# Kernel optimization log

Measured on AMD Instinct MI355X. Metric: run time of the kernel, lower is better.

The kernel has to match this reference:

```python
import jax, jax.numpy as jnp
import numpy as np
import math

D_MODEL = 1024
N_HEADS = 16
D_K = 64
D_V = 64
B = 4
S = 1024


def setup_inputs() -> dict:
    key = jax.random.key(0)
    ks = jax.random.split(key, 11)
    # xavier-ish init scale for projections
    s_in = 1.0 / math.sqrt(D_MODEL)
    return {
        "queries": jax.random.normal(ks[0], (B, S, D_MODEL), jnp.float32),
        "keys": jax.random.normal(ks[1], (B, S, D_MODEL), jnp.float32),
        "values": jax.random.normal(ks[2], (B, S, D_MODEL), jnp.float32),
        "Wq": jax.random.normal(ks[3], (D_MODEL, N_HEADS * D_K), jnp.float32) * s_in,
        "bq": jnp.zeros((N_HEADS * D_K,), jnp.float32),
        "Wk": jax.random.normal(ks[4], (D_MODEL, N_HEADS * D_K), jnp.float32) * s_in,
        "bk": jnp.zeros((N_HEADS * D_K,), jnp.float32),
        "Wv": jax.random.normal(ks[5], (D_MODEL, N_HEADS * D_V), jnp.float32) * s_in,
        "bv": jnp.zeros((N_HEADS * D_V,), jnp.float32),
        "Wo": jax.random.normal(ks[6], (N_HEADS * D_V, D_MODEL), jnp.float32) * (1.0 / math.sqrt(N_HEADS * D_V)),
        "bo": jnp.zeros((D_MODEL,), jnp.float32),
    }


def reference(queries, keys, values, Wq, bq, Wk, bk, Wv, bv, Wo, bo):
    Bq, Sq, _ = queries.shape
    Sk = keys.shape[1]
    scale = 1.0 / math.sqrt(D_K)
    # projections -> [B, S, H, d]
    q = (queries @ Wq + bq).reshape(Bq, Sq, N_HEADS, D_K)
    k = (keys @ Wk + bk).reshape(Bq, Sk, N_HEADS, D_K)
    v = (values @ Wv + bv).reshape(Bq, Sk, N_HEADS, D_V)
    # scaled dot-product attention: scores [B, H, Sq, Sk]
    scores = jnp.einsum("bqhd,bkhd->bhqk", q, k) * scale
    attn = jax.nn.softmax(scores, axis=-1)
    # weighted values -> [B, Sq, H*D_V]
    out = jnp.einsum("bhqk,bkhd->bqhd", attn, v).reshape(Bq, Sq, N_HEADS * D_V)
    return out @ Wo + bo
```

## Files before the change

### kernel.cpp

```cpp
#include <hip/hip_runtime.h>
#include <hip/hip_bf16.h>

typedef __attribute__((ext_vector_type(4))) float f32x4;
typedef __attribute__((ext_vector_type(16))) float f32x16;
typedef __attribute__((ext_vector_type(8))) short bf16x8;
typedef __attribute__((ext_vector_type(4))) unsigned short u16x4;
typedef __attribute__((ext_vector_type(8))) unsigned short u16x8;
typedef __attribute__((ext_vector_type(2))) unsigned int u32x2;

#define MFMA16(a, b, c) __builtin_amdgcn_mfma_f32_16x16x32_bf16((a), (b), (c), 0, 0, 0)
#define MFMA32(a, b, c) __builtin_amdgcn_mfma_f32_32x32x16_bf16((a), (b), (c), 0, 0, 0)

static __device__ __forceinline__ unsigned short f2bf(float f) {
    union { float f; unsigned int u; } v; v.f = f;
    unsigned int r = v.u + 0x7FFFu + ((v.u >> 16) & 1u);
    return (unsigned short)(r >> 16);
}
static __device__ __forceinline__ unsigned int pk2(float x, float y) {
    unsigned int r;
    asm("v_cvt_pk_bf16_f32 %0, %1, %2" : "=v"(r) : "v"(x), "v"(y));
    return r;
}

static __device__ __forceinline__ void gload_lds16(const void* g, void* l) {
    __builtin_amdgcn_global_load_lds(
        (const __attribute__((address_space(1))) void*)g,
        (__attribute__((address_space(3))) void*)l, 16, 0, 0);
}

__global__ __launch_bounds__(256) void convert_act(
    const float* __restrict__ q, const float* __restrict__ k,
    const float* __restrict__ v, unsigned short* __restrict__ qc,
    unsigned short* __restrict__ kc, unsigned short* __restrict__ vc) {
    const float* src = blockIdx.y == 0 ? q : (blockIdx.y == 1 ? k : v);
    unsigned short* dst = blockIdx.y == 0 ? qc : (blockIdx.y == 1 ? kc : vc);
    size_t off = ((size_t)blockIdx.x * 256 + threadIdx.x) * 8;
    f32x4 a = *(const f32x4*)&src[off];
    f32x4 b = *(const f32x4*)&src[off + 4];
    union { unsigned int u[4]; u16x8 v; } o;
    o.u[0] = pk2(a[0], a[1]); o.u[1] = pk2(a[2], a[3]);
    o.u[2] = pk2(b[0], b[1]); o.u[3] = pk2(b[2], b[3]);
    *(u16x8*)&dst[off] = o.v;
}

__global__ __launch_bounds__(256) void transpose_w(
    const float* __restrict__ Wq, const float* __restrict__ Wk,
    const float* __restrict__ Wv, const float* __restrict__ Wo,
    unsigned short* __restrict__ Wt_all, unsigned short* __restrict__ Wot) {
    __shared__ unsigned short T[64][65];
    const int z = blockIdx.z;
    const float* W = z == 0 ? Wq : (z == 1 ? Wk : (z == 2 ? Wv : Wo));
    unsigned short* Wt = z < 3 ? (Wt_all + (size_t)z * 1024 * 1024) : Wot;
    const int k0 = blockIdx.y * 64, n0 = blockIdx.x * 64;
    const int t = threadIdx.x;
    const int rl = t >> 4, c4 = (t & 15) * 4;
#pragma unroll
    for (int i = 0; i < 4; ++i) {
        f32x4 v = *(const f32x4*)&W[(size_t)(k0 + rl + 16 * i) * 1024 + n0 + c4];
#pragma unroll
        for (int j = 0; j < 4; ++j) T[rl + 16 * i][c4 + j] = f2bf(v[j]);
    }
    __syncthreads();
#pragma unroll
    for (int i = 0; i < 4; ++i) {
        u16x4 o;
#pragma unroll
        for (int j = 0; j < 4; ++j) o[j] = T[c4 + j][rl + 16 * i];
        *(u16x4*)&Wt[(size_t)(n0 + rl + 16 * i) * 1024 + k0 + c4] = o;
    }
}

template <bool OUT_BF16, int BN>
__global__ __launch_bounds__(256, 2) void gemm_fast(
    const unsigned short* __restrict__ A0, const unsigned short* __restrict__ A1,
    const unsigned short* __restrict__ A2, const unsigned short* __restrict__ Wt,
    const float* __restrict__ b0, const float* __restrict__ b1,
    const float* __restrict__ b2, void* __restrict__ Outv, int ldo) {
    constexpr int NF = BN / 32;
    __shared__ __align__(16) unsigned short As[128 * 32];
    __shared__ __align__(16) unsigned short Bs[BN * 32];

    const int t = threadIdx.x;
    const int w = t >> 6, lane = t & 63;
    const int wr = w >> 1, wc = w & 1;
    const int g = lane >> 4, r15 = lane & 15;
    const int bm = blockIdx.y * 128;
    const int bn = blockIdx.x * BN;
    const int msel = bn >> 10;
    const unsigned short* A = msel == 0 ? A0 : (msel == 1 ? A1 : A2);
    const float* bias = msel == 0 ? b0 : (msel == 1 ? b1 : b2);
    const int l4 = lane >> 2, c8 = (lane & 3) * 8;

    f32x4 acc[4][NF];
#pragma unroll
    for (int m = 0; m < 4; ++m)
#pragma unroll
        for (int n = 0; n < NF; ++n) acc[m][n] = (f32x4){0.f, 0.f, 0.f, 0.f};

    for (int kt = 0; kt < 1024; kt += 32) {
        __syncthreads();
        gload_lds16(&A[(size_t)(bm + 16 * w + l4) * 1024 + kt + c8], &As[w * 512]);
        gload_lds16(&A[(size_t)(bm + 16 * (w + 4) + l4) * 1024 + kt + c8], &As[(w + 4) * 512]);
        if (BN == 128) {
            gload_lds16(&Wt[(size_t)(bn + 16 * w + l4) * 1024 + kt + c8], &Bs[w * 512]);
            gload_lds16(&Wt[(size_t)(bn + 16 * (w + 4) + l4) * 1024 + kt + c8],
                        &Bs[(w + 4) * 512 % (BN * 32)]);
        } else {
            gload_lds16(&Wt[(size_t)(bn + 16 * w + l4) * 1024 + kt + c8], &Bs[w * 512]);
        }
        __syncthreads();
        bf16x8 af[4], bfr[NF];
#pragma unroll
        for (int m = 0; m < 4; ++m)
            af[m] = *(const bf16x8*)&As[(wr * 64 + m * 16 + r15) * 32 + g * 8];
#pragma unroll
        for (int n = 0; n < NF; ++n)
            bfr[n] = *(const bf16x8*)&Bs[(wc * (BN / 2) + n * 16 + r15) * 32 + g * 8];
#pragma unroll
        for (int m = 0; m < 4; ++m)
#pragma unroll
            for (int n = 0; n < NF; ++n)
                acc[m][n] = MFMA16(af[m], bfr[n], acc[m][n]);
    }

    float* Of = (float*)Outv;
    unsigned short* Ob = (unsigned short*)Outv;
#pragma unroll
    for (int n = 0; n < NF; ++n) {
        int col = bn + wc * (BN / 2) + n * 16 + r15;
        float bv = bias[col & 1023];
#pragma unroll
        for (int m = 0; m < 4; ++m) {
#pragma unroll
            for (int r = 0; r < 4; ++r) {
                int row = bm + wr * 64 + m * 16 + g * 4 + r;
                float val = acc[m][n][r] + bv;
                if (OUT_BF16)
                    Ob[(size_t)row * ldo + col] = f2bf(val);
                else
                    Of[(size_t)row * ldo + col] = val;
            }
        }
    }
}

template <bool A_BF16, bool OUT_BF16>
__global__ __launch_bounds__(256, 2) void gemm_kernel(
    const void* __restrict__ Av, const float* __restrict__ W,
    const float* __restrict__ bias, void* __restrict__ Outv) {
    __shared__ __align__(16) unsigned short As[128][40];
    __shared__ __align__(16) unsigned short Bs[128][40];

    const int t = threadIdx.x;
    const int bm = blockIdx.y * 128;
    const int bn = blockIdx.x * 128;
    const int w = t >> 6, lane = t & 63;
    const int wr = w >> 1, wc = w & 1;
    const int g = lane >> 4, r15 = lane & 15;

    f32x4 acc[4][4];
#pragma unroll
    for (int m = 0; m < 4; ++m)
#pragma unroll
        for (int n = 0; n < 4; ++n) acc[m][n] = (f32x4){0.f, 0.f, 0.f, 0.f};

    const float* Af = (const float*)Av;
    const unsigned short* Ab = (const unsigned short*)Av;

    for (int kt = 0; kt < 1024; kt += 32) {
        __syncthreads();
#pragma unroll
        for (int i = 0; i < 4; ++i) {
            int row = (t >> 3) + i * 32;
            int c4 = (t & 7) * 4;
            if (A_BF16) {
                u16x4 v = *(const u16x4*)&Ab[(size_t)(bm + row) * 1024 + kt + c4];
                *(u16x4*)&As[row][c4] = v;
            } else {
                f32x4 v = *(const f32x4*)&Af[(size_t)(bm + row) * 1024 + kt + c4];
                u16x4 o;
                o[0] = f2bf(v[0]); o[1] = f2bf(v[1]);
                o[2] = f2bf(v[2]); o[3] = f2bf(v[3]);
                *(u16x4*)&As[row][c4] = o;
            }
        }
#pragma unroll
        for (int i = 0; i < 4; ++i) {
            int k = (t >> 5) + i * 8;
            int c4 = (t & 31) * 4;
            f32x4 v = *(const f32x4*)&W[(size_t)(kt + k) * 1024 + bn + c4];
#pragma unroll
            for (int j = 0; j < 4; ++j) Bs[c4 + j][k] = f2bf(v[j]);
        }
        __syncthreads();
        bf16x8 af[4], bfr[4];
#pragma unroll
        for (int m = 0; m < 4; ++m)
            af[m] = *(const bf16x8*)&As[wr * 64 + m * 16 + r15][g * 8];
#pragma unroll
        for (int n = 0; n < 4; ++n)
            bfr[n] = *(const bf16x8*)&Bs[wc * 64 + n * 16 + r15][g * 8];
#pragma unroll
        for (int m = 0; m < 4; ++m)
#pragma unroll
            for (int n = 0; n < 4; ++n)
                acc[m][n] = MFMA16(af[m], bfr[n], acc[m][n]);
    }

    float* Of = (float*)Outv;
    unsigned short* Ob = (unsigned short*)Outv;
#pragma unroll
    for (int n = 0; n < 4; ++n) {
        int col = bn + wc * 64 + n * 16 + r15;
        float bv = bias[col];
#pragma unroll
        for (int m = 0; m < 4; ++m) {
#pragma unroll
            for (int r = 0; r < 4; ++r) {
                int row = bm + wr * 64 + m * 16 + g * 4 + r;
                float val = acc[m][n][r] + bv;
                if (OUT_BF16)
                    Ob[(size_t)row * 1024 + col] = f2bf(val);
                else
                    Of[(size_t)row * 1024 + col] = val;
            }
        }
    }
}

__global__ __launch_bounds__(256, 2) void attn32_kernel(
    const unsigned short* __restrict__ Q, const unsigned short* __restrict__ K,
    const unsigned short* __restrict__ V, unsigned short* __restrict__ O, int ld) {
    __shared__ __align__(16) unsigned short Kls[2][64 * 80];
    __shared__ __align__(16) unsigned short Vls[2][64 * 80];

    const int t = threadIdx.x;
    const int w = t >> 6, lane = t & 63;
    const int q5 = lane & 31, hi = lane >> 5;

    const int id = blockIdx.x;
    const int sid = (id & 7) * 64 + (id >> 3);
    const int bh = sid >> 3, qb = sid & 7;
    const int b = bh >> 4, h = bh & 15;
    const int brow = b * 1024;
    const int q0 = qb * 128;

    const float c2 = 0.18033688f;

    const unsigned short* Qrow = Q + (size_t)(brow + q0 + w * 32 + q5) * ld + h * 64;
    bf16x8 qreg[8];
#pragma unroll
    for (int j = 0; j < 8; ++j) qreg[j] = *(const bf16x8*)&Qrow[8 * j];
    bf16x8 qsel[4];
#pragma unroll
    for (int kk = 0; kk < 4; ++kk) qsel[kk] = hi ? qreg[2 * kk + 1] : qreg[2 * kk];

    const int krow = t >> 2, kpart = t & 3;
    const int vp = t & 31, vdc = t >> 5;
    const unsigned short* Kg = K + h * 64;
    const unsigned short* Vg = V + h * 64;

    u16x8 kr0, kr1, vr0, vr1;
#define STG_LOAD(KT)                                                            \
    {                                                                           \
        size_t kro = (size_t)(brow + (KT) + krow) * ld;                         \
        kr0 = *(const u16x8*)&Kg[kro + kpart * 8];                              \
        kr1 = *(const u16x8*)&Kg[kro + kpart * 8 + 32];                         \
        size_t vro = (size_t)(brow + (KT) + 2 * vp) * ld;                       \
        vr0 = *(const u16x8*)&Vg[vro + vdc * 8];                                \
        vr1 = *(const u16x8*)&Vg[vro + ld + vdc * 8];                           \
    }
#define STG_WRITE(BUF)                                                          \
    {                                                                           \
        char* kb_ = (char*)Kls[BUF];                                            \
        int tg_ = (krow & 7) << 4;                                              \
        *(u16x8*)(kb_ + krow * 160 + ((kpart * 16) ^ tg_)) = kr0;               \
        *(u16x8*)(kb_ + krow * 160 + (((kpart + 4) * 16) ^ tg_)) = kr1;         \
        char* vb_ = (char*)Vls[BUF];                                            \
        _Pragma("unroll") for (int j_ = 0; j_ < 8; ++j_) {                      \
            int d_ = vdc * 8 + j_;                                              \
            unsigned int pk_ = (unsigned int)(unsigned short)vr0[j_] |          \
                               ((unsigned int)(unsigned short)vr1[j_] << 16);   \
            *(unsigned int*)(vb_ + d_ * 160 + ((vp * 4) ^ ((d_ & 7) << 4)))     \
                = pk_;                                                          \
        }                                                                       \
    }

    f32x16 acc0 = {}, acc1 = {};
    float mrun = -1e30f, lrun = 0.f;

    STG_LOAD(0);
    STG_WRITE(0);
    __syncthreads();

    int cur = 0;
    for (int tile = 0; tile < 16; ++tile) {
        const bool more = tile < 15;
        if (more) STG_LOAD(tile * 64 + 64);

        char* kb = (char*)Kls[cur];
        f32x16 st0 = {}, st1 = {};
        {
            const int tg0 = (q5 & 7) << 4;
            char* kp0 = kb + q5 * 160;
            char* kp1 = kb + (q5 + 32) * 160;
            __builtin_amdgcn_s_setprio(1);
#pragma unroll
            for (int kk = 0; kk < 4; ++kk) {
                int so = ((2 * kk + hi) * 16) ^ tg0;
                bf16x8 kf0 = *(const bf16x8*)(kp0 + so);
                bf16x8 kf1 = *(const bf16x8*)(kp1 + so);
                st0 = MFMA32(kf0, qsel[kk], st0);
                st1 = MFMA32(kf1, qsel[kk], st1);
            }
            __builtin_amdgcn_s_setprio(0);
        }

        float mloc = fmaxf(st0[0], st0[1]);
#pragma unroll
        for (int r = 2; r < 16; ++r) mloc = fmaxf(mloc, st0[r]);
#pragma unroll
        for (int r = 0; r < 16; ++r) mloc = fmaxf(mloc, st1[r]);
        mloc = fmaxf(mloc, __shfl_xor(mloc, 32));
        if (!__all(mloc - mrun <= 64.f)) {
            float mnew = fmaxf(mrun, mloc);
            float sf = exp2f((mrun - mnew) * c2);
            mrun = mnew;
            lrun *= sf;
#pragma unroll
            for (int r = 0; r < 16; ++r) { acc0[r] *= sf; acc1[r] *= sf; }
        }
        float mneg = -mrun * c2;
        float rs = 0.f;
#pragma unroll
        for (int r = 0; r < 16; ++r) {
            st0[r] = exp2f(fmaf(st0[r], c2, mneg));
            rs += st0[r];
        }
#pragma unroll
        for (int r = 0; r < 16; ++r) {
            st1[r] = exp2f(fmaf(st1[r], c2, mneg));
            rs += st1[r];
        }
        rs += __shfl_xor(rs, 32);
        lrun += rs;

        char* vb = (char*)Vls[cur];
        const int tgv = (q5 & 7) << 4;
        char* vp0 = vb + q5 * 160;
        char* vp1 = vb + (q5 + 32) * 160;
        __builtin_amdgcn_s_setprio(1);
#define PV_HALF(ST, CT)                                                         \
    _Pragma("unroll") for (int ks = 0; ks < 2; ++ks) {                          \
        unsigned int a0 = pk2(ST[8 * ks + 0], ST[8 * ks + 1]);                  \
        unsigned int a1 = pk2(ST[8 * ks + 2], ST[8 * ks + 3]);                  \
        unsigned int a2 = pk2(ST[8 * ks + 4], ST[8 * ks + 5]);                  \
        unsigned int a3 = pk2(ST[8 * ks + 6], ST[8 * ks + 7]);                  \
        unsigned int x0 = __shfl_xor(a0, 32), x1 = __shfl_xor(a1, 32);          \
        unsigned int x2 = __shfl_xor(a2, 32), x3 = __shfl_xor(a3, 32);          \
        union { unsigned int u[4]; bf16x8 v; } pfu;                             \
        pfu.u[0] = hi ? x2 : a0;                                                \
        pfu.u[1] = hi ? x3 : a1;                                                \
        pfu.u[2] = hi ? a2 : x0;                                                \
        pfu.u[3] = hi ? a3 : x1;                                                \
        int co = ((32 * (2 * (CT) + ks) + 16 * hi)) ^ tgv;                      \
        bf16x8 vf0 = *(const bf16x8*)(vp0 + co);                                \
        bf16x8 vf1 = *(const bf16x8*)(vp1 + co);                                \
        acc0 = MFMA32(vf0, pfu.v, acc0);                                        \
        acc1 = MFMA32(vf1, pfu.v, acc1);                                        \
    }
        PV_HALF(st0, 0);
        PV_HALF(st1, 1);
        __builtin_amdgcn_s_setprio(0);

        if (more) STG_WRITE(cur ^ 1);
        __syncthreads();
        cur ^= 1;
    }

    const float inv = 1.0f / lrun;
    unsigned short* Orow = O + (size_t)(brow + q0 + w * 32 + q5) * 1024 + h * 64;
#pragma unroll
    for (int k = 0; k < 4; ++k) {
        int d0 = 8 * k + 4 * hi;
        u32x2 pa, pb;
        pa[0] = pk2(acc0[4 * k + 0] * inv, acc0[4 * k + 1] * inv);
        pa[1] = pk2(acc0[4 * k + 2] * inv, acc0[4 * k + 3] * inv);
        *(u32x2*)&Orow[d0] = pa;
        pb[0] = pk2(acc1[4 * k + 0] * inv, acc1[4 * k + 1] * inv);
        pb[1] = pk2(acc1[4 * k + 2] * inv, acc1[4 * k + 3] * inv);
        *(u32x2*)&Orow[32 + d0] = pb;
    }
#undef STG_LOAD
#undef STG_WRITE
#undef PV_HALF
}

extern "C" void kernel_launch(void* const* d_in, const int* in_sizes, int n_in,
                              void* d_out, int out_size, void* d_ws, size_t ws_size,
                              hipStream_t stream) {
    const float* q  = (const float*)d_in[0];
    const float* k  = (const float*)d_in[1];
    const float* v  = (const float*)d_in[2];
    const float* Wq = (const float*)d_in[3];
    const float* bq = (const float*)d_in[4];
    const float* Wk = (const float*)d_in[5];
    const float* bk = (const float*)d_in[6];
    const float* Wv = (const float*)d_in[7];
    const float* bv = (const float*)d_in[8];
    const float* Wo = (const float*)d_in[9];
    const float* bo = (const float*)d_in[10];

    const size_t M1 = (size_t)1024 * 1024;
    const size_t NEED = 28 * M1 * sizeof(unsigned short);

    dim3 bt(256, 1, 1);
    if (ws_size >= NEED) {
        unsigned short* qc  = (unsigned short*)d_ws;
        unsigned short* kc  = qc + 4 * M1;
        unsigned short* vc  = kc + 4 * M1;
        unsigned short* Wt  = vc + 4 * M1;
        unsigned short* Wot = Wt + 3 * M1;
        unsigned short* QKV = Wot + M1;
        unsigned short* Ob  = qc;

        convert_act<<<dim3(2048, 3), bt, 0, stream>>>(q, k, v, qc, kc, vc);
        transpose_w<<<dim3(16, 16, 4), bt, 0, stream>>>(Wq, Wk, Wv, Wo, Wt, Wot);
        gemm_fast<true, 128><<<dim3(24, 32), bt, 0, stream>>>(qc, kc, vc, Wt, bq, bk, bv, QKV, 3072);
        attn32_kernel<<<dim3(512), bt, 0, stream>>>(QKV, QKV + 1024, QKV + 2048, Ob, 3072);
        gemm_fast<false, 64><<<dim3(16, 32), bt, 0, stream>>>(Ob, Ob, Ob, Wot, bo, bo, bo, d_out, 1024);
    } else {
        const size_t NE = (size_t)4096 * 1024;
        unsigned short* Qb = (unsigned short*)d_ws;
        unsigned short* Kb = Qb + NE;
        unsigned short* Vb = Kb + NE;
        unsigned short* Ob = Vb + NE;
        dim3 gg(8, 32);
        gemm_kernel<false, true><<<gg, bt, 0, stream>>>(q, Wq, bq, Qb);
        gemm_kernel<false, true><<<gg, bt, 0, stream>>>(k, Wk, bk, Kb);
        gemm_kernel<false, true><<<gg, bt, 0, stream>>>(v, Wv, bv, Vb);
        attn32_kernel<<<dim3(512), bt, 0, stream>>>(Qb, Kb, Vb, Ob, 1024);
        gemm_kernel<true, false><<<gg, bt, 0, stream>>>(Ob, Wo, bo, d_out);
    }
}
```

Before: 217.6 us.

## Split attention over KV halves with merge, double-buffer GEMMs, fuse prepass kernels

Fuses activation conversion and weight transpose into one prepass launch. Double-buffers the GEMM LDS staging so the next K-tile loads while the current one computes, adds MFMA priority hints, and retiles the output projection to BM=64 rows and 128 columns. Splits attention across two KV halves to double the grid to 1024 blocks, writing partial outputs plus max/sum stats that a new merge kernel combines. The split adds an extra launch, extra memory traffic and a second bf16 rounding of the partial outputs, and the small-workspace fallback path is removed.

```diff
diff --git a/kernel.cpp b/kernel.cpp
--- a/kernel.cpp
+++ b/kernel.cpp
@@ -21,6 +21,9 @@
     asm("v_cvt_pk_bf16_f32 %0, %1, %2" : "=v"(r) : "v"(x), "v"(y));
     return r;
 }
+static __device__ __forceinline__ float bf2f(unsigned short u) {
+    return __uint_as_float((unsigned int)u << 16);
+}
 
 static __device__ __forceinline__ void gload_lds16(const void* g, void* l) {
     __builtin_amdgcn_global_load_lds(
@@ -28,112 +31,126 @@
         (__attribute__((address_space(3))) void*)l, 16, 0, 0);
 }
 
-__global__ __launch_bounds__(256) void convert_act(
+__global__ __launch_bounds__(256) void prepass(
     const float* __restrict__ q, const float* __restrict__ k,
-    const float* __restrict__ v, unsigned short* __restrict__ qc,
-    unsigned short* __restrict__ kc, unsigned short* __restrict__ vc) {
-    const float* src = blockIdx.y == 0 ? q : (blockIdx.y == 1 ? k : v);
-    unsigned short* dst = blockIdx.y == 0 ? qc : (blockIdx.y == 1 ? kc : vc);
-    size_t off = ((size_t)blockIdx.x * 256 + threadIdx.x) * 8;
-    f32x4 a = *(const f32x4*)&src[off];
-    f32x4 b = *(const f32x4*)&src[off + 4];
-    union { unsigned int u[4]; u16x8 v; } o;
-    o.u[0] = pk2(a[0], a[1]); o.u[1] = pk2(a[2], a[3]);
-    o.u[2] = pk2(b[0], b[1]); o.u[3] = pk2(b[2], b[3]);
-    *(u16x8*)&dst[off] = o.v;
-}
-
-__global__ __launch_bounds__(256) void transpose_w(
-    const float* __restrict__ Wq, const float* __restrict__ Wk,
-    const float* __restrict__ Wv, const float* __restrict__ Wo,
-    unsigned short* __restrict__ Wt_all, unsigned short* __restrict__ Wot) {
+    const float* __restrict__ v, const float* __restrict__ Wq,
+    const float* __restrict__ Wk, const float* __restrict__ Wv,
+    const float* __restrict__ Wo, unsigned short* __restrict__ qc,
+    unsigned short* __restrict__ kc, unsigned short* __restrict__ vc,
+    unsigned short* __restrict__ Wt, unsigned short* __restrict__ Wot) {
     __shared__ unsigned short T[64][65];
-    const int z = blockIdx.z;
-    const float* W = z == 0 ? Wq : (z == 1 ? Wk : (z == 2 ? Wv : Wo));
-    unsigned short* Wt = z < 3 ? (Wt_all + (size_t)z * 1024 * 1024) : Wot;
-    const int k0 = blockIdx.y * 64, n0 = blockIdx.x * 64;
-    const int t = threadIdx.x;
-    const int rl = t >> 4, c4 = (t & 15) * 4;
-#pragma unroll
-    for (int i = 0; i < 4; ++i) {
-        f32x4 v = *(const f32x4*)&W[(size_t)(k0 + rl + 16 * i) * 1024 + n0 + c4];
-#pragma unroll
-        for (int j = 0; j < 4; ++j) T[rl + 16 * i][c4 + j] = f2bf(v[j]);
-    }
-    __syncthreads();
-#pragma unroll
-    for (int i = 0; i < 4; ++i) {
-        u16x4 o;
-#pragma unroll
-        for (int j = 0; j < 4; ++j) o[j] = T[c4 + j][rl + 16 * i];
-        *(u16x4*)&Wt[(size_t)(n0 + rl + 16 * i) * 1024 + k0 + c4] = o;
-    }
-}
-
-template <bool OUT_BF16, int BN>
+    const int id = blockIdx.x, t = threadIdx.x;
+    if (id < 6144) {
+        const int z = id >> 11;
+        const float* src = z == 0 ? q : (z == 1 ? k : v);
+        unsigned short* dst = z == 0 ? qc : (z == 1 ? kc : vc);
+        size_t off = ((size_t)(id & 2047) * 256 + t) * 8;
+        f32x4 a = *(const f32x4*)&src[off];
+        f32x4 b = *(const f32x4*)&src[off + 4];
+        union { unsigned int u[4]; u16x8 v; } o;
+        o.u[0] = pk2(a[0], a[1]); o.u[1] = pk2(a[2], a[3]);
+        o.u[2] = pk2(b[0], b[1]); o.u[3] = pk2(b[2], b[3]);
+        *(u16x8*)&dst[off] = o.v;
+    } else {
+        int r = id - 6144;
+        const int z = r >> 8; r &= 255;
+        const float* W = z == 0 ? Wq : (z == 1 ? Wk : (z == 2 ? Wv : Wo));
+        unsigned short* Wd = z < 3 ? (Wt + (size_t)z * 1024 * 1024) : Wot;
+        const int k0 = (r >> 4) * 64, n0 = (r & 15) * 64;
+        const int rl = t >> 4, c4 = (t & 15) * 4;
+#pragma unroll
+        for (int i = 0; i < 4; ++i) {
+            f32x4 vv = *(const f32x4*)&W[(size_t)(k0 + rl + 16 * i) * 1024 + n0 + c4];
+#pragma unroll
+            for (int j = 0; j < 4; ++j) T[rl + 16 * i][c4 + j] = f2bf(vv[j]);
+        }
+        __syncthreads();
+#pragma unroll
+        for (int i = 0; i < 4; ++i) {
+            u16x4 o;
+#pragma unroll
+            for (int j = 0; j < 4; ++j) o[j] = T[c4 + j][rl + 16 * i];
+            *(u16x4*)&Wd[(size_t)(n0 + rl + 16 * i) * 1024 + k0 + c4] = o;
+        }
+    }
+}
+
+template <bool OUT_BF16, int BM>
 __global__ __launch_bounds__(256, 2) void gemm_fast(
     const unsigned short* __restrict__ A0, const unsigned short* __restrict__ A1,
     const unsigned short* __restrict__ A2, const unsigned short* __restrict__ Wt,
     const float* __restrict__ b0, const float* __restrict__ b1,
     const float* __restrict__ b2, void* __restrict__ Outv, int ldo) {
-    constexpr int NF = BN / 32;
-    __shared__ __align__(16) unsigned short As[128 * 32];
-    __shared__ __align__(16) unsigned short Bs[BN * 32];
+    constexpr int MF = BM / 32;
+    __shared__ __align__(16) unsigned short As[2][BM * 32];
+    __shared__ __align__(16) unsigned short Bs[2][128 * 32];
 
     const int t = threadIdx.x;
     const int w = t >> 6, lane = t & 63;
     const int wr = w >> 1, wc = w & 1;
     const int g = lane >> 4, r15 = lane & 15;
-    const int bm = blockIdx.y * 128;
-    const int bn = blockIdx.x * BN;
+    const int bm = blockIdx.y * BM;
+    const int bn = blockIdx.x * 128;
     const int msel = bn >> 10;
     const unsigned short* A = msel == 0 ? A0 : (msel == 1 ? A1 : A2);
     const float* bias = msel == 0 ? b0 : (msel == 1 ? b1 : b2);
     const int l4 = lane >> 2, c8 = (lane & 3) * 8;
 
-    f32x4 acc[4][NF];
-#pragma unroll
-    for (int m = 0; m < 4; ++m)
-#pragma unroll
-        for (int n = 0; n < NF; ++n) acc[m][n] = (f32x4){0.f, 0.f, 0.f, 0.f};
-
+    f32x4 acc[MF][4];
+#pragma unroll
+    for (int m = 0; m < MF; ++m)
+#pragma unroll
+        for (int n = 0; n < 4; ++n) acc[m][n] = (f32x4){0.f, 0.f, 0.f, 0.f};
+
+#define G_STAGE(BUF, KT)                                                          \
+    {                                                                             \
+        gload_lds16(&A[(size_t)(bm + 16 * w + l4) * 1024 + (KT) + c8],            \
+                    &As[BUF][w * 512]);                                           \
+        if (BM == 128)                                                            \
+            gload_lds16(&A[(size_t)(bm + 16 * (w + 4) + l4) * 1024 + (KT) + c8],  \
+                        &As[BUF][((w + 4) * 512) % (BM * 32)]);                   \
+        gload_lds16(&Wt[(size_t)(bn + 16 * w + l4) * 1024 + (KT) + c8],           \
+                    &Bs[BUF][w * 512]);                                           \
+        gload_lds16(&Wt[(size_t)(bn + 16 * (w + 4) + l4) * 1024 + (KT) + c8],     \
+                    &Bs[BUF][(w + 4) * 512]);                                     \
+    }
+
+    G_STAGE(0, 0);
+    __syncthreads();
+
+    int cur = 0;
     for (int kt = 0; kt < 1024; kt += 32) {
+        if (kt < 992) G_STAGE(cur ^ 1, kt + 32);
+        bf16x8 af[MF], bfr[4];
+#pragma unroll
+        for (int m = 0; m < MF; ++m)
+            af[m] = *(const bf16x8*)&As[cur][(wr * (BM / 2) + m * 16 + r15) * 32 + g * 8];
+#pragma unroll
+        for (int n = 0; n < 4; ++n)
+            bfr[n] = *(const bf16x8*)&Bs[cur][(wc * 64 + n * 16 + r15) * 32 + g * 8];
+        __builtin_amdgcn_s_setprio(1);
+#pragma unroll
+        for (int m = 0; m < MF; ++m)
+#pragma unroll
+            for (int n = 0; n < 4; ++n)
+                acc[m][n] = MFMA16(af[m], bfr[n], acc[m][n]);
+        __builtin_amdgcn_s_setprio(0);
         __syncthreads();
-        gload_lds16(&A[(size_t)(bm + 16 * w + l4) * 1024 + kt + c8], &As[w * 512]);
-        gload_lds16(&A[(size_t)(bm + 16 * (w + 4) + l4) * 1024 + kt + c8], &As[(w + 4) * 512]);
-        if (BN == 128) {
-            gload_lds16(&Wt[(size_t)(bn + 16 * w + l4) * 1024 + kt + c8], &Bs[w * 512]);
-            gload_lds16(&Wt[(size_t)(bn + 16 * (w + 4) + l4) * 1024 + kt + c8],
-                        &Bs[(w + 4) * 512 % (BN * 32)]);
-        } else {
-            gload_lds16(&Wt[(size_t)(bn + 16 * w + l4) * 1024 + kt + c8], &Bs[w * 512]);
-        }
-        __syncthreads();
-        bf16x8 af[4], bfr[NF];
-#pragma unroll
-        for (int m = 0; m < 4; ++m)
-            af[m] = *(const bf16x8*)&As[(wr * 64 + m * 16 + r15) * 32 + g * 8];
-#pragma unroll
-        for (int n = 0; n < NF; ++n)
-            bfr[n] = *(const bf16x8*)&Bs[(wc * (BN / 2) + n * 16 + r15) * 32 + g * 8];
-#pragma unroll
-        for (int m = 0; m < 4; ++m)
-#pragma unroll
-            for (int n = 0; n < NF; ++n)
-                acc[m][n] = MFMA16(af[m], bfr[n], acc[m][n]);
-    }
+        cur ^= 1;
+    }
+#undef G_STAGE
 
     float* Of = (float*)Outv;
     unsigned short* Ob = (unsigned short*)Outv;
 #pragma unroll
-    for (int n = 0; n < NF; ++n) {
-        int col = bn + wc * (BN / 2) + n * 16 + r15;
+    for (int n = 0; n < 4; ++n) {
+        int col = bn + wc * 64 + n * 16 + r15;
         float bv = bias[col & 1023];
 #pragma unroll
-        for (int m = 0; m < 4; ++m) {
+        for (int m = 0; m < MF; ++m) {
 #pragma unroll
             for (int r = 0; r < 4; ++r) {
-                int row = bm + wr * 64 + m * 16 + g * 4 + r;
+                int row = bm + wr * (BM / 2) + m * 16 + g * 4 + r;
                 float val = acc[m][n][r] + bv;
                 if (OUT_BF16)
                     Ob[(size_t)row * ldo + col] = f2bf(val);
@@ -144,93 +161,10 @@
     }
 }
 
-template <bool A_BF16, bool OUT_BF16>
-__global__ __launch_bounds__(256, 2) void gemm_kernel(
-    const void* __restrict__ Av, const float* __restrict__ W,
-    const float* __restrict__ bias, void* __restrict__ Outv) {
-    __shared__ __align__(16) unsigned short As[128][40];
-    __shared__ __align__(16) unsigned short Bs[128][40];
-
-    const int t = threadIdx.x;
-    const int bm = blockIdx.y * 128;
-    const int bn = blockIdx.x * 128;
-    const int w = t >> 6, lane = t & 63;
-    const int wr = w >> 1, wc = w & 1;
-    const int g = lane >> 4, r15 = lane & 15;
-
-    f32x4 acc[4][4];
-#pragma unroll
-    for (int m = 0; m < 4; ++m)
-#pragma unroll
-        for (int n = 0; n < 4; ++n) acc[m][n] = (f32x4){0.f, 0.f, 0.f, 0.f};
-
-    const float* Af = (const float*)Av;
-    const unsigned short* Ab = (const unsigned short*)Av;
-
-    for (int kt = 0; kt < 1024; kt += 32) {
-        __syncthreads();
-#pragma unroll
-        for (int i = 0; i < 4; ++i) {
-            int row = (t >> 3) + i * 32;
-            int c4 = (t & 7) * 4;
-            if (A_BF16) {
-                u16x4 v = *(const u16x4*)&Ab[(size_t)(bm + row) * 1024 + kt + c4];
-                *(u16x4*)&As[row][c4] = v;
-            } else {
-                f32x4 v = *(const f32x4*)&Af[(size_t)(bm + row) * 1024 + kt + c4];
-                u16x4 o;
-                o[0] = f2bf(v[0]); o[1] = f2bf(v[1]);
-                o[2] = f2bf(v[2]); o[3] = f2bf(v[3]);
-                *(u16x4*)&As[row][c4] = o;
-            }
-        }
-#pragma unroll
-        for (int i = 0; i < 4; ++i) {
-            int k = (t >> 5) + i * 8;
-            int c4 = (t & 31) * 4;
-            f32x4 v = *(const f32x4*)&W[(size_t)(kt + k) * 1024 + bn + c4];
-#pragma unroll
-            for (int j = 0; j < 4; ++j) Bs[c4 + j][k] = f2bf(v[j]);
-        }
-        __syncthreads();
-        bf16x8 af[4], bfr[4];
-#pragma unroll
-        for (int m = 0; m < 4; ++m)
-            af[m] = *(const bf16x8*)&As[wr * 64 + m * 16 + r15][g * 8];
-#pragma unroll
-        for (int n = 0; n < 4; ++n)
-            bfr[n] = *(const bf16x8*)&Bs[wc * 64 + n * 16 + r15][g * 8];
-#pragma unroll
-        for (int m = 0; m < 4; ++m)
-#pragma unroll
-            for (int n = 0; n < 4; ++n)
-                acc[m][n] = MFMA16(af[m], bfr[n], acc[m][n]);
-    }
-
-    float* Of = (float*)Outv;
-    unsigned short* Ob = (unsigned short*)Outv;
-#pragma unroll
-    for (int n = 0; n < 4; ++n) {
-        int col = bn + wc * 64 + n * 16 + r15;
-        float bv = bias[col];
-#pragma unroll
-        for (int m = 0; m < 4; ++m) {
-#pragma unroll
-            for (int r = 0; r < 4; ++r) {
-                int row = bm + wr * 64 + m * 16 + g * 4 + r;
-                float val = acc[m][n][r] + bv;
-                if (OUT_BF16)
-                    Ob[(size_t)row * 1024 + col] = f2bf(val);
-                else
-                    Of[(size_t)row * 1024 + col] = val;
-            }
-        }
-    }
-}
-
-__global__ __launch_bounds__(256, 2) void attn32_kernel(
+__global__ __launch_bounds__(256, 4) void attn32_kernel(
     const unsigned short* __restrict__ Q, const unsigned short* __restrict__ K,
-    const unsigned short* __restrict__ V, unsigned short* __restrict__ O, int ld) {
+    const unsigned short* __restrict__ V, unsigned short* __restrict__ Opart,
+    float* __restrict__ ML, int ld) {
     __shared__ __align__(16) unsigned short Kls[2][64 * 80];
     __shared__ __align__(16) unsigned short Vls[2][64 * 80];
 
@@ -239,11 +173,13 @@
     const int q5 = lane & 31, hi = lane >> 5;
 
     const int id = blockIdx.x;
-    const int sid = (id & 7) * 64 + (id >> 3);
-    const int bh = sid >> 3, qb = sid & 7;
+    const int sid = (id & 7) * 128 + (id >> 3);
+    const int bh = sid >> 4, sub = sid & 15;
+    const int qb = sub >> 1, half = sub & 1;
     const int b = bh >> 4, h = bh & 15;
     const int brow = b * 1024;
     const int q0 = qb * 128;
+    const int kv0 = half * 512;
 
     const float c2 = 0.18033688f;
 
@@ -289,14 +225,14 @@
     f32x16 acc0 = {}, acc1 = {};
     float mrun = -1e30f, lrun = 0.f;
 
-    STG_LOAD(0);
+    STG_LOAD(kv0);
     STG_WRITE(0);
     __syncthreads();
 
     int cur = 0;
-    for (int tile = 0; tile < 16; ++tile) {
-        const bool more = tile < 15;
-        if (more) STG_LOAD(tile * 64 + 64);
+    for (int tile = 0; tile < 8; ++tile) {
+        const bool more = tile < 7;
+        if (more) STG_LOAD(kv0 + tile * 64 + 64);
 
         char* kb = (char*)Kls[cur];
         f32x16 st0 = {}, st1 = {};
@@ -378,8 +314,10 @@
         cur ^= 1;
     }
 
+    const int grow = brow + q0 + w * 32 + q5;
     const float inv = 1.0f / lrun;
-    unsigned short* Orow = O + (size_t)(brow + q0 + w * 32 + q5) * 1024 + h * 64;
+    unsigned short* Orow =
+        Opart + (size_t)half * 4194304 + (size_t)grow * 1024 + h * 64;
 #pragma unroll
     for (int k = 0; k < 4; ++k) {
         int d0 = 8 * k + 4 * hi;
@@ -391,9 +329,37 @@
         pb[1] = pk2(acc1[4 * k + 2] * inv, acc1[4 * k + 3] * inv);
         *(u32x2*)&Orow[32 + d0] = pb;
     }
+    if (hi == 0)
+        ((float2*)ML)[half * 65536 + grow * 16 + h] = make_float2(mrun, lrun);
 #undef STG_LOAD
 #undef STG_WRITE
 #undef PV_HALF
+}
+
+__global__ __launch_bounds__(256) void attn_merge(
+    const unsigned short* __restrict__ Opart, const float* __restrict__ ML,
+    unsigned short* __restrict__ Omg) {
+    const float c2 = 0.18033688f;
+    const int gid = blockIdx.x * 256 + threadIdx.x;
+    const int pair = gid >> 3;
+    const int dp = gid & 7;
+    const int row = pair >> 4, h = pair & 15;
+    const float2 ml0 = ((const float2*)ML)[pair];
+    const float2 ml1 = ((const float2*)ML)[65536 + pair];
+    float mn = fmaxf(ml0.x, ml1.x);
+    float w0 = ml0.y * exp2f((ml0.x - mn) * c2);
+    float w1 = ml1.y * exp2f((ml1.x - mn) * c2);
+    float inv = 1.0f / (w0 + w1);
+    w0 *= inv; w1 *= inv;
+    size_t off = (size_t)row * 1024 + h * 64 + dp * 8;
+    u16x8 a = *(const u16x8*)&Opart[off];
+    u16x8 b = *(const u16x8*)&Opart[4194304 + off];
+    union { unsigned int u[4]; u16x8 v; } o;
+#pragma unroll
+    for (int j = 0; j < 4; ++j)
+        o.u[j] = pk2(bf2f(a[2 * j]) * w0 + bf2f(b[2 * j]) * w1,
+                     bf2f(a[2 * j + 1]) * w0 + bf2f(b[2 * j + 1]) * w1);
+    *(u16x8*)&Omg[off] = o.v;
 }
 
 extern "C" void kernel_launch(void* const* d_in, const int* in_sizes, int n_in,
@@ -412,34 +378,24 @@
     const float* bo = (const float*)d_in[10];
 
     const size_t M1 = (size_t)1024 * 1024;
-    const size_t NEED = 28 * M1 * sizeof(unsigned short);
+    unsigned short* qc  = (unsigned short*)d_ws;
+    unsigned short* kc  = qc + 4 * M1;
+    unsigned short* vc  = kc + 4 * M1;
+    unsigned short* Wt  = vc + 4 * M1;
+    unsigned short* Wot = Wt + 3 * M1;
+    unsigned short* QKV = Wot + M1;
+    unsigned short* Opart = qc;
+    float* ML = (float*)vc;
+    unsigned short* Omg = QKV;
 
     dim3 bt(256, 1, 1);
-    if (ws_size >= NEED) {
-        unsigned short* qc  = (unsigned short*)d_ws;
-        unsigned short* kc  = qc + 4 * M1;
-        unsigned short* vc  = kc + 4 * M1;
-        unsigned short* Wt  = vc + 4 * M1;
-        unsigned short* Wot = Wt + 3 * M1;
-        unsigned short* QKV = Wot + M1;
-        unsigned short* Ob  = qc;
-
-        convert_act<<<dim3(2048, 3), bt, 0, stream>>>(q, k, v, qc, kc, vc);
-        transpose_w<<<dim3(16, 16, 4), bt, 0, stream>>>(Wq, Wk, Wv, Wo, Wt, Wot);
-        gemm_fast<true, 128><<<dim3(24, 32), bt, 0, stream>>>(qc, kc, vc, Wt, bq, bk, bv, QKV, 3072);
-        attn32_kernel<<<dim3(512), bt, 0, stream>>>(QKV, QKV + 1024, QKV + 2048, Ob, 3072);
-        gemm_fast<false, 64><<<dim3(16, 32), bt, 0, stream>>>(Ob, Ob, Ob, Wot, bo, bo, bo, d_out, 1024);
-    } else {
-        const size_t NE = (size_t)4096 * 1024;
-        unsigned short* Qb = (unsigned short*)d_ws;
-        unsigned short* Kb = Qb + NE;
-        unsigned short* Vb = Kb + NE;
-        unsigned short* Ob = Vb + NE;
-        dim3 gg(8, 32);
-        gemm_kernel<false, true><<<gg, bt, 0, stream>>>(q, Wq, bq, Qb);
-        gemm_kernel<false, true><<<gg, bt, 0, stream>>>(k, Wk, bk, Kb);
-        gemm_kernel<false, true><<<gg, bt, 0, stream>>>(v, Wv, bv, Vb);
-        attn32_kernel<<<dim3(512), bt, 0, stream>>>(Qb, Kb, Vb, Ob, 1024);
-        gemm_kernel<true, false><<<gg, bt, 0, stream>>>(Ob, Wo, bo, d_out);
-    }
-}
+    prepass<<<dim3(7168), bt, 0, stream>>>(q, k, v, Wq, Wk, Wv, Wo,
+                                           qc, kc, vc, Wt, Wot);
+    gemm_fast<true, 128><<<dim3(24, 32), bt, 0, stream>>>(
+        qc, kc, vc, Wt, bq, bk, bv, QKV, 3072);
+    attn32_kernel<<<dim3(1024), bt, 0, stream>>>(
+        QKV, QKV + 1024, QKV + 2048, Opart, ML, 3072);
+    attn_merge<<<dim3(2048), bt, 0, stream>>>(Opart, ML, Omg);
+    gemm_fast<false, 64><<<dim3(8, 64), bt, 0, stream>>>(
+        Omg, Omg, Omg, Wot, bo, bo, bo, d_out, 1024);
+}
```

New measurement: 232.9 us. 7.1% more time.
